# Optimization experiments

Hardware: AMD Instinct MI355X
Metric: run time of the kernel (lower is better)

## Reference

```python
import jax, jax.numpy as jnp
import numpy as np

N, E = 50000, 800000
IN_C, HID, OUT_C, HEADS = 256, 32, 16, 8
NEG_SLOPE = 0.2


def gat_conv(x, edge_index, W, att_src, att_dst, bias, heads, out_c, concat):
    """PyG-style GATConv (inference, dropout off, add_self_loops=True).

    x: [N, F_in], edge_index: [2, E] with row0=src(j), row1=dst(i).
    W: [F_in, heads*out_c], att_src/att_dst: [heads, out_c], bias: [heads*out_c] or [out_c].
    """
    n = x.shape[0]
    loops = jnp.arange(n, dtype=edge_index.dtype)
    src = jnp.concatenate([edge_index[0], loops])
    dst = jnp.concatenate([edge_index[1], loops])

    xl = (x @ W).reshape(n, heads, out_c)              # [N, H, C]
    a_src = jnp.einsum('nhc,hc->nh', xl, att_src)      # [N, H]
    a_dst = jnp.einsum('nhc,hc->nh', xl, att_dst)

    e = a_src[src] + a_dst[dst]                        # [E', H]
    e = jnp.where(e >= 0, e, NEG_SLOPE * e)            # leaky_relu
    e_max = jax.ops.segment_max(e, dst, num_segments=n)
    e_exp = jnp.exp(e - e_max[dst])
    denom = jax.ops.segment_sum(e_exp, dst, num_segments=n)
    alpha = e_exp / (denom[dst] + 1e-16)               # segment softmax over in-edges of dst

    msg = alpha[:, :, None] * xl[src]                  # [E', H, C]
    out = jax.ops.segment_sum(msg, dst, num_segments=n)  # [N, H, C]
    if concat:
        out = out.reshape(n, heads * out_c)
    else:
        out = out.mean(axis=1)
    return out + bias


def setup_inputs() -> dict:
    key = jax.random.key(0)
    ks = jax.random.split(key, 10)
    s_in = 1.0 / np.sqrt(IN_C)
    s_h = 1.0 / np.sqrt(HEADS * HID)
    x = jax.random.normal(ks[0], (N, IN_C), dtype=jnp.float32)
    edge_index = jax.random.randint(ks[1], (2, E), 0, N, dtype=jnp.int64)
    return {
        'x': x,
        'edge_index': edge_index,
        'W1': jax.random.normal(ks[2], (IN_C, HEADS * HID), dtype=jnp.float32) * s_in,
        'att_src1': jax.random.normal(ks[3], (HEADS, HID), dtype=jnp.float32) * s_h,
        'att_dst1': jax.random.normal(ks[4], (HEADS, HID), dtype=jnp.float32) * s_h,
        'b1': jnp.zeros((HEADS * HID,), dtype=jnp.float32),
        'W2': jax.random.normal(ks[5], (HEADS * HID, OUT_C), dtype=jnp.float32) * s_h,
        'att_src2': jax.random.normal(ks[6], (1, OUT_C), dtype=jnp.float32) * 0.1,
        'att_dst2': jax.random.normal(ks[7], (1, OUT_C), dtype=jnp.float32) * 0.1,
        'b2': jnp.zeros((OUT_C,), dtype=jnp.float32),
    }


def reference(x, edge_index, W1, att_src1, att_dst1, b1, W2, att_src2, att_dst2, b2):
    h = gat_conv(x, edge_index, W1, att_src1, att_dst1, b1, HEADS, HID, concat=True)
    h = jax.nn.relu(h)
    # F.dropout(training=False) is identity at inference
    out = gat_conv(h, edge_index, W2, att_src2, att_dst2, b2, 1, OUT_C, concat=False)
    return jax.nn.log_softmax(out, axis=1)
```

## Files before the change

### kernel.cpp

```cpp
#include <hip/hip_runtime.h>

#define IN_C 256
#define H1 8
#define C1 32
#define F1 256
#define OC 16
#define NEG 0.2f

typedef short short8 __attribute__((ext_vector_type(8)));
typedef unsigned short ushort8 __attribute__((ext_vector_type(8)));
typedef float floatx4 __attribute__((ext_vector_type(4)));

__device__ __forceinline__ unsigned short f2bf(float f) {
    unsigned u = __builtin_bit_cast(unsigned, f);
    u = (u + 0x7fffu + ((u >> 16) & 1u)) >> 16;
    return (unsigned short)u;
}
__device__ __forceinline__ float bf2f(unsigned short h) {
    unsigned u = ((unsigned)h) << 16;
    return __builtin_bit_cast(float, u);
}

__global__ __launch_bounds__(256) void k_fuse0(const int* __restrict__ ei,
                                               int* __restrict__ cnt,
                                               const float* __restrict__ W1,
                                               const float* __restrict__ W2,
                                               unsigned short* __restrict__ w1t,
                                               unsigned short* __restrict__ w2t, int E)
{
    int gid = blockIdx.x * 256 + threadIdx.x;
    if (gid < E) atomicAdd(&cnt[ei[E + gid]], 1);
    if (gid < 65536) {
        int n = gid >> 8, k = gid & 255;
        w1t[n * 256 + k] = f2bf(W1[k * 256 + n]);
    } else if (gid < 65536 + 4096) {
        int r = gid - 65536;
        int n = r >> 8, k = r & 255;
        w2t[n * 256 + k] = f2bf(W2[k * 16 + n]);
    }
}

__global__ __launch_bounds__(256) void k_gemm1(const float* __restrict__ A,
                                               const unsigned short* __restrict__ Bt,
                                               unsigned short* __restrict__ Cb, int M)
{
    __shared__ short As[128][40];
    __shared__ short Bs[128][40];
    const int tid  = threadIdx.x;
    const int lane = tid & 63;
    const int w    = tid >> 6;
    const int bm   = blockIdx.x * 128;
    const int bn   = blockIdx.y * 128;
    const int wm   = (w >> 1) * 64;
    const int wn   = (w & 1) * 64;
    const int srow = tid >> 1;
    const int soff = (tid & 1) * 16;
    floatx4 acc[4][4] = {};
    for (int k0 = 0; k0 < 256; k0 += 32) {
        __syncthreads();
        {
            int gr = bm + srow;
            float4 f0 = {0,0,0,0}, f1 = {0,0,0,0}, f2 = {0,0,0,0}, f3 = {0,0,0,0};
            if (gr < M) {
                const float4* p = (const float4*)(A + (size_t)gr * 256 + k0 + soff);
                f0 = p[0]; f1 = p[1]; f2 = p[2]; f3 = p[3];
            }
            ushort8 v0, v1;
            v0[0]=f2bf(f0.x); v0[1]=f2bf(f0.y); v0[2]=f2bf(f0.z); v0[3]=f2bf(f0.w);
            v0[4]=f2bf(f1.x); v0[5]=f2bf(f1.y); v0[6]=f2bf(f1.z); v0[7]=f2bf(f1.w);
            v1[0]=f2bf(f2.x); v1[1]=f2bf(f2.y); v1[2]=f2bf(f2.z); v1[3]=f2bf(f2.w);
            v1[4]=f2bf(f3.x); v1[5]=f2bf(f3.y); v1[6]=f2bf(f3.z); v1[7]=f2bf(f3.w);
            *(ushort8*)&As[srow][soff]     = v0;
            *(ushort8*)&As[srow][soff + 8] = v1;
        }
        {
            const ushort8* p = (const ushort8*)(Bt + (size_t)(bn + srow) * 256 + k0 + soff);
            *(ushort8*)&Bs[srow][soff]     = p[0];
            *(ushort8*)&Bs[srow][soff + 8] = p[1];
        }
        __syncthreads();
        short8 af[4], bf[4];
        const int q8 = (lane >> 4) * 8;
        const int l15 = lane & 15;
#pragma unroll
        for (int i = 0; i < 4; ++i) af[i] = *(const short8*)&As[wm + i * 16 + l15][q8];
#pragma unroll
        for (int j = 0; j < 4; ++j) bf[j] = *(const short8*)&Bs[wn + j * 16 + l15][q8];
#pragma unroll
        for (int i = 0; i < 4; ++i)
#pragma unroll
            for (int j = 0; j < 4; ++j)
                acc[i][j] = __builtin_amdgcn_mfma_f32_16x16x32_bf16(af[i], bf[j], acc[i][j], 0, 0, 0);
    }
    const int l15 = lane & 15;
    const int rq  = (lane >> 4) * 4;
#pragma unroll
    for (int i = 0; i < 4; ++i) {
#pragma unroll
        for (int reg = 0; reg < 4; ++reg) {
            int gr = bm + wm + i * 16 + rq + reg;
            if (gr < M) {
#pragma unroll
                for (int j = 0; j < 4; ++j)
                    Cb[(size_t)gr * 256 + bn + wn + j * 16 + l15] = f2bf(acc[i][j][reg]);
            }
        }
    }
}

__global__ __launch_bounds__(256) void k_att1(const unsigned short* __restrict__ xl,
                                              const float* __restrict__ att_s,
                                              const float* __restrict__ att_d,
                                              float* __restrict__ asrc,
                                              float* __restrict__ adst, int N)
{
    int idx = blockIdx.x * 256 + threadIdx.x;
    if (idx >= N * H1) return;
    int i = idx >> 3, h = idx & 7;
    const ushort4* xr = (const ushort4*)(xl + (size_t)i * F1 + h * C1);
    const float* s = att_s + h * C1;
    const float* d = att_d + h * C1;
    float s1 = 0.f, s2 = 0.f;
#pragma unroll
    for (int c4 = 0; c4 < 8; ++c4) {
        ushort4 v = xr[c4];
        float f0 = bf2f(v.x), f1 = bf2f(v.y), f2 = bf2f(v.z), f3 = bf2f(v.w);
        int c = c4 * 4;
        s1 += f0 * s[c] + f1 * s[c+1] + f2 * s[c+2] + f3 * s[c+3];
        s2 += f0 * d[c] + f1 * d[c+1] + f2 * d[c+2] + f3 * d[c+3];
    }
    asrc[idx] = s1; adst[idx] = s2;
}

__global__ __launch_bounds__(256) void k_scan_a(const int* __restrict__ cnt,
                                                int* __restrict__ rp,
                                                int* __restrict__ bsum, int N)
{
    __shared__ int ws4[4];
    int t = threadIdx.x, lane = t & 63, wid = t >> 6;
    int i = blockIdx.x * 256 + t;
    int v = (i < N) ? cnt[i] : 0;
    int incl = v;
#pragma unroll
    for (int off = 1; off < 64; off <<= 1) {
        int tv = __shfl_up(incl, off, 64);
        if (lane >= off) incl += tv;
    }
    if (lane == 63) ws4[wid] = incl;
    __syncthreads();
    int add = 0;
    for (int w = 0; w < wid; ++w) add += ws4[w];
    incl += add;
    if (i < N) rp[i + 1] = incl;
    if (t == 255) bsum[blockIdx.x] = incl;
}

__global__ __launch_bounds__(256) void k_scan_b(const int* __restrict__ bsum,
                                                int* __restrict__ boff, int NB)
{
    __shared__ int ws4[4];
    int t = threadIdx.x, lane = t & 63, wid = t >> 6;
    int i0 = t * 4;
    int v[4];
#pragma unroll
    for (int k = 0; k < 4; ++k) { int i = i0 + k; v[k] = (i < NB) ? bsum[i] : 0; }
    int s = v[0] + v[1] + v[2] + v[3];
    int incl = s;
#pragma unroll
    for (int off = 1; off < 64; off <<= 1) {
        int tv = __shfl_up(incl, off, 64);
        if (lane >= off) incl += tv;
    }
    if (lane == 63) ws4[wid] = incl;
    __syncthreads();
    int wpre = 0;
    for (int w = 0; w < wid; ++w) wpre += ws4[w];
    int run = wpre + incl - s;
#pragma unroll
    for (int k = 0; k < 4; ++k) {
        int i = i0 + k;
        if (i < NB) boff[i] = run;
        run += v[k];
    }
}

__global__ __launch_bounds__(256) void k_scan_c(int* __restrict__ rp,
                                                const int* __restrict__ boff,
                                                const int* __restrict__ cnt,
                                                int* __restrict__ cur, int N)
{
    int i = blockIdx.x * 256 + threadIdx.x;
    if (i < N) {
        int v = rp[i + 1] + boff[blockIdx.x];
        rp[i + 1] = v;
        cur[i] = v - cnt[i];
    }
    if (i == 0) rp[0] = 0;
}

__global__ __launch_bounds__(256) void k_scatter(const int* __restrict__ ei,
                                                 int* __restrict__ cur,
                                                 int* __restrict__ ssrc, int E)
{
    int e = blockIdx.x * 256 + threadIdx.x;
    if (e >= E) return;
    int s = ei[e];
    int d = ei[E + e];
    int pos = atomicAdd(&cur[d], 1);
    ssrc[pos] = s;
}

__global__ __launch_bounds__(256) void k_gather1(const int* __restrict__ rp,
                                                 const int* __restrict__ ssrc,
                                                 const unsigned short* __restrict__ xl,
                                                 const float* __restrict__ asrc,
                                                 const float* __restrict__ adst,
                                                 const float* __restrict__ bias,
                                                 unsigned short* __restrict__ hout, int N)
{
    int lane = threadIdx.x & 63;
    int node = blockIdx.x * 4 + (threadIdx.x >> 6);
    if (node >= N) return;
    int h  = lane >> 3;
    int cb = lane * 4;
    float ad = adst[(size_t)node * H1 + h];
    float e = asrc[(size_t)node * H1 + h] + ad;
    e = e >= 0.f ? e : NEG * e;
    float w = __expf(e);
    ushort4 xv = *(const ushort4*)(xl + (size_t)node * F1 + cb);
    float ax = w * bf2f(xv.x), ay = w * bf2f(xv.y), az = w * bf2f(xv.z), aw = w * bf2f(xv.w);
    float den = w;
    int jb = rp[node], je = rp[node + 1];
    int j = jb;
    for (; j + 4 <= je; j += 4) {
        int s0 = ssrc[j], s1 = ssrc[j+1], s2 = ssrc[j+2], s3 = ssrc[j+3];
        float e0 = asrc[(size_t)s0 * H1 + h] + ad;
        float e1 = asrc[(size_t)s1 * H1 + h] + ad;
        float e2 = asrc[(size_t)s2 * H1 + h] + ad;
        float e3 = asrc[(size_t)s3 * H1 + h] + ad;
        ushort4 r0 = *(const ushort4*)(xl + (size_t)s0 * F1 + cb);
        ushort4 r1 = *(const ushort4*)(xl + (size_t)s1 * F1 + cb);
        ushort4 r2 = *(const ushort4*)(xl + (size_t)s2 * F1 + cb);
        ushort4 r3 = *(const ushort4*)(xl + (size_t)s3 * F1 + cb);
        e0 = e0 >= 0.f ? e0 : NEG * e0;  float w0 = __expf(e0);
        e1 = e1 >= 0.f ? e1 : NEG * e1;  float w1 = __expf(e1);
        e2 = e2 >= 0.f ? e2 : NEG * e2;  float w2 = __expf(e2);
        e3 = e3 >= 0.f ? e3 : NEG * e3;  float w3 = __expf(e3);
        den += w0 + w1 + w2 + w3;
        ax += w0*bf2f(r0.x) + w1*bf2f(r1.x) + w2*bf2f(r2.x) + w3*bf2f(r3.x);
        ay += w0*bf2f(r0.y) + w1*bf2f(r1.y) + w2*bf2f(r2.y) + w3*bf2f(r3.y);
        az += w0*bf2f(r0.z) + w1*bf2f(r1.z) + w2*bf2f(r2.z) + w3*bf2f(r3.z);
        aw += w0*bf2f(r0.w) + w1*bf2f(r1.w) + w2*bf2f(r2.w) + w3*bf2f(r3.w);
    }
    for (; j < je; ++j) {
        int s = ssrc[j];
        float ev = asrc[(size_t)s * H1 + h] + ad;
        ev = ev >= 0.f ? ev : NEG * ev;
        float wv = __expf(ev);
        ushort4 sv = *(const ushort4*)(xl + (size_t)s * F1 + cb);
        ax += wv * bf2f(sv.x); ay += wv * bf2f(sv.y);
        az += wv * bf2f(sv.z); aw += wv * bf2f(sv.w);
        den += wv;
    }
    float inv = 1.f / (den + 1e-16f);
    float4 bv = *(const float4*)(bias + cb);
    ushort4 o;
    o.x = f2bf(fmaxf(ax * inv + bv.x, 0.f));
    o.y = f2bf(fmaxf(ay * inv + bv.y, 0.f));
    o.z = f2bf(fmaxf(az * inv + bv.z, 0.f));
    o.w = f2bf(fmaxf(aw * inv + bv.w, 0.f));
    *(ushort4*)(hout + (size_t)node * F1 + cb) = o;
}

__global__ __launch_bounds__(256) void k_gemm2(const unsigned short* __restrict__ Hm,
                                               const unsigned short* __restrict__ W2t,
                                               const float* __restrict__ as2,
                                               const float* __restrict__ ad2,
                                               unsigned short* __restrict__ xl2b,
                                               float* __restrict__ asrc,
                                               float* __restrict__ adst, int N)
{
    const int lane = threadIdx.x & 63;
    const int wid  = threadIdx.x >> 6;
    const int rowbase = blockIdx.x * 64 + wid * 16;
    const int col = lane & 15;
    const int q8  = (lane >> 4) * 8;
    const int m   = rowbase + col;
    const bool mv = m < N;
    const unsigned short* arow = Hm + (size_t)m * 256 + q8;
    const unsigned short* brow = W2t + (size_t)col * 256 + q8;
    floatx4 acc = {0.f, 0.f, 0.f, 0.f};
#pragma unroll
    for (int t = 0; t < 8; ++t) {
        short8 af = {0,0,0,0,0,0,0,0};
        if (mv) af = *(const short8*)(arow + t * 32);
        short8 bf = *(const short8*)(brow + t * 32);
        acc = __builtin_amdgcn_mfma_f32_16x16x32_bf16(af, bf, acc, 0, 0, 0);
    }
    float s_as = as2[col], s_ad = ad2[col];
    const int rq = (lane >> 4) * 4;
#pragma unroll
    for (int reg = 0; reg < 4; ++reg) {
        int row = rowbase + rq + reg;
        float v = acc[reg];
        float s1 = v * s_as, s2 = v * s_ad;
#pragma unroll
        for (int o = 1; o < 16; o <<= 1) { s1 += __shfl_xor(s1, o, 16); s2 += __shfl_xor(s2, o, 16); }
        if (row < N) {
            xl2b[(size_t)row * OC + col] = f2bf(v);
            if (col == 0) { asrc[row] = s1; adst[row] = s2; }
        }
    }
}

__global__ __launch_bounds__(256) void k_gather2(const int* __restrict__ rp,
                                                 const int* __restrict__ ssrc,
                                                 const unsigned short* __restrict__ xl2b,
                                                 const float* __restrict__ asrc,
                                                 const float* __restrict__ adst,
                                                 const float* __restrict__ bias,
                                                 float* __restrict__ out, int N)
{
    int sub  = threadIdx.x & 15;
    int node = blockIdx.x * 16 + (threadIdx.x >> 4);
    if (node >= N) return;
    float ad = adst[node];
    float e = asrc[node] + ad;
    e = e >= 0.f ? e : NEG * e;
    float w = __expf(e);
    float acc = w * bf2f(xl2b[(size_t)node * OC + sub]);
    float den = w;
    int jb = rp[node], je = rp[node + 1];
    int j = jb;
    for (; j + 4 <= je; j += 4) {
        int s0 = ssrc[j], s1i = ssrc[j+1], s2i = ssrc[j+2], s3i = ssrc[j+3];
        float e0 = asrc[s0] + ad, e1 = asrc[s1i] + ad, e2 = asrc[s2i] + ad, e3 = asrc[s3i] + ad;
        float v0 = bf2f(xl2b[(size_t)s0 * OC + sub]);
        float v1 = bf2f(xl2b[(size_t)s1i * OC + sub]);
        float v2 = bf2f(xl2b[(size_t)s2i * OC + sub]);
        float v3 = bf2f(xl2b[(size_t)s3i * OC + sub]);
        e0 = e0 >= 0.f ? e0 : NEG * e0;  float w0 = __expf(e0);
        e1 = e1 >= 0.f ? e1 : NEG * e1;  float w1 = __expf(e1);
        e2 = e2 >= 0.f ? e2 : NEG * e2;  float w2 = __expf(e2);
        e3 = e3 >= 0.f ? e3 : NEG * e3;  float w3 = __expf(e3);
        den += w0 + w1 + w2 + w3;
        acc += w0 * v0 + w1 * v1 + w2 * v2 + w3 * v3;
    }
    for (; j < je; ++j) {
        int s = ssrc[j];
        float ev = asrc[s] + ad;
        ev = ev >= 0.f ? ev : NEG * ev;
        float wv = __expf(ev);
        acc += wv * bf2f(xl2b[(size_t)s * OC + sub]);
        den += wv;
    }
    float v = acc / (den + 1e-16f) + bias[sub];
    float m = v;
#pragma unroll
    for (int o = 1; o < 16; o <<= 1) m = fmaxf(m, __shfl_xor(m, o, 16));
    float ex = __expf(v - m);
    float ss = ex;
#pragma unroll
    for (int o = 1; o < 16; o <<= 1) ss += __shfl_xor(ss, o, 16);
    out[(size_t)node * OC + sub] = v - m - logf(ss);
}

extern "C" void kernel_launch(void* const* d_in, const int* in_sizes, int n_in,
                              void* d_out, int out_size, void* d_ws, size_t ws_size,
                              hipStream_t stream)
{
    const float* x   = (const float*)d_in[0];
    const int*   ei  = (const int*)d_in[1];
    const float* W1  = (const float*)d_in[2];
    const float* as1 = (const float*)d_in[3];
    const float* ad1 = (const float*)d_in[4];
    const float* b1  = (const float*)d_in[5];
    const float* W2  = (const float*)d_in[6];
    const float* as2 = (const float*)d_in[7];
    const float* ad2 = (const float*)d_in[8];
    const float* b2  = (const float*)d_in[9];
    float* out = (float*)d_out;

    const int N = in_sizes[0] / IN_C;
    const int E = in_sizes[1] / 2;
    const int NB = (N + 255) / 256;

    char* base = (char*)d_ws;
    unsigned short* xl1b = (unsigned short*)base;
    unsigned short* hb   = xl1b + (size_t)N * F1;
    unsigned short* w1t  = hb + (size_t)N * F1;
    unsigned short* w2t  = w1t + 256 * 256;
    unsigned short* xl2b = w2t + 16 * 256;
    float* asrc1 = (float*)(xl2b + (size_t)N * OC);
    float* adst1 = asrc1 + (size_t)N * H1;
    float* asrc2 = adst1 + (size_t)N * H1;
    float* adst2 = asrc2 + N;
    int*   rp    = (int*)(adst2 + N);
    int*   cnt   = rp + (N + 1);
    int*   cur   = cnt + N;
    int*   bsum  = cur + N;
    int*   boff  = bsum + 1024;
    int*   ssrc  = boff + 1024;

    hipMemsetAsync(cnt, 0, (size_t)N * sizeof(int), stream);
    k_fuse0<<<(E + 255) / 256, 256, 0, stream>>>(ei, cnt, W1, W2, w1t, w2t, E);
    k_scan_a<<<NB, 256, 0, stream>>>(cnt, rp, bsum, N);
    k_scan_b<<<1, 256, 0, stream>>>(bsum, boff, NB);
    k_scan_c<<<NB, 256, 0, stream>>>(rp, boff, cnt, cur, N);
    k_scatter<<<(E + 255) / 256, 256, 0, stream>>>(ei, cur, ssrc, E);

    k_gemm1<<<dim3((N + 127) / 128, 2), 256, 0, stream>>>(x, w1t, xl1b, N);
    k_att1<<<(N * H1 + 255) / 256, 256, 0, stream>>>(xl1b, as1, ad1, asrc1, adst1, N);
    k_gather1<<<(N + 3) / 4, 256, 0, stream>>>(rp, ssrc, xl1b, asrc1, adst1, b1, hb, N);

    k_gemm2<<<(N + 63) / 64, 256, 0, stream>>>(hb, w2t, as2, ad2, xl2b, asrc2, adst2, N);
    k_gather2<<<(N + 15) / 16, 256, 0, stream>>>(rp, ssrc, xl2b, asrc2, adst2, b2, out, N);
}
```

Before: 333.5 us.

## Fuse attention-score dots into GEMM1 epilogue and split gather1 edges across half-waves

Drops the separate k_att1 kernel. The per-head source and destination attention dot products are now computed in the GEMM1 epilogue from fp32 accumulators, reduced with 16-lane xor shuffles, so the bf16 xl1 matrix is not re-read. Separately, gather1 now gives each half-wave alternate edges, with each lane loading 8 bf16 values (16 bytes) instead of 4, and combines the two halves with a cross-half shuffle at the end. This trades more epilogue shuffles and half-idle lanes on short neighbor lists for fewer kernel launches and wider, more parallel gather loads.

```diff
diff --git a/kernel.cpp b/kernel.cpp
--- a/kernel.cpp
+++ b/kernel.cpp
@@ -42,7 +42,11 @@
 
 __global__ __launch_bounds__(256) void k_gemm1(const float* __restrict__ A,
                                                const unsigned short* __restrict__ Bt,
-                                               unsigned short* __restrict__ Cb, int M)
+                                               const float* __restrict__ att_s,
+                                               const float* __restrict__ att_d,
+                                               unsigned short* __restrict__ Cb,
+                                               float* __restrict__ asrc,
+                                               float* __restrict__ adst, int M)
 {
     __shared__ short As[128][40];
     __shared__ short Bs[128][40];
@@ -81,11 +85,11 @@
         __syncthreads();
         short8 af[4], bf[4];
         const int q8 = (lane >> 4) * 8;
-        const int l15 = lane & 15;
-#pragma unroll
-        for (int i = 0; i < 4; ++i) af[i] = *(const short8*)&As[wm + i * 16 + l15][q8];
-#pragma unroll
-        for (int j = 0; j < 4; ++j) bf[j] = *(const short8*)&Bs[wn + j * 16 + l15][q8];
+        const int l15i = lane & 15;
+#pragma unroll
+        for (int i = 0; i < 4; ++i) af[i] = *(const short8*)&As[wm + i * 16 + l15i][q8];
+#pragma unroll
+        for (int j = 0; j < 4; ++j) bf[j] = *(const short8*)&Bs[wn + j * 16 + l15i][q8];
 #pragma unroll
         for (int i = 0; i < 4; ++i)
 #pragma unroll
@@ -94,42 +98,37 @@
     }
     const int l15 = lane & 15;
     const int rq  = (lane >> 4) * 4;
+    const int hA = (bn + wn) >> 5;
+    const int hB = hA + 1;
+    const float aS_A0 = att_s[hA * 32 + l15],      aS_A1 = att_s[hA * 32 + 16 + l15];
+    const float aS_B0 = att_s[hB * 32 + l15],      aS_B1 = att_s[hB * 32 + 16 + l15];
+    const float aD_A0 = att_d[hA * 32 + l15],      aD_A1 = att_d[hA * 32 + 16 + l15];
+    const float aD_B0 = att_d[hB * 32 + l15],      aD_B1 = att_d[hB * 32 + 16 + l15];
 #pragma unroll
     for (int i = 0; i < 4; ++i) {
 #pragma unroll
         for (int reg = 0; reg < 4; ++reg) {
             int gr = bm + wm + i * 16 + rq + reg;
+            float sA = acc[i][0][reg] * aS_A0 + acc[i][1][reg] * aS_A1;
+            float dA = acc[i][0][reg] * aD_A0 + acc[i][1][reg] * aD_A1;
+            float sB = acc[i][2][reg] * aS_B0 + acc[i][3][reg] * aS_B1;
+            float dB = acc[i][2][reg] * aD_B0 + acc[i][3][reg] * aD_B1;
+#pragma unroll
+            for (int o = 1; o < 16; o <<= 1) {
+                sA += __shfl_xor(sA, o, 16);  dA += __shfl_xor(dA, o, 16);
+                sB += __shfl_xor(sB, o, 16);  dB += __shfl_xor(dB, o, 16);
+            }
             if (gr < M) {
 #pragma unroll
                 for (int j = 0; j < 4; ++j)
                     Cb[(size_t)gr * 256 + bn + wn + j * 16 + l15] = f2bf(acc[i][j][reg]);
+                if (l15 == 0) {
+                    asrc[(size_t)gr * H1 + hA] = sA;  adst[(size_t)gr * H1 + hA] = dA;
+                    asrc[(size_t)gr * H1 + hB] = sB;  adst[(size_t)gr * H1 + hB] = dB;
+                }
             }
         }
     }
-}
-
-__global__ __launch_bounds__(256) void k_att1(const unsigned short* __restrict__ xl,
-                                              const float* __restrict__ att_s,
-                                              const float* __restrict__ att_d,
-                                              float* __restrict__ asrc,
-                                              float* __restrict__ adst, int N)
-{
-    int idx = blockIdx.x * 256 + threadIdx.x;
-    if (idx >= N * H1) return;
-    int i = idx >> 3, h = idx & 7;
-    const ushort4* xr = (const ushort4*)(xl + (size_t)i * F1 + h * C1);
-    const float* s = att_s + h * C1;
-    const float* d = att_d + h * C1;
-    float s1 = 0.f, s2 = 0.f;
-#pragma unroll
-    for (int c4 = 0; c4 < 8; ++c4) {
-        ushort4 v = xr[c4];
-        float f0 = bf2f(v.x), f1 = bf2f(v.y), f2 = bf2f(v.z), f3 = bf2f(v.w);
-        int c = c4 * 4;
-        s1 += f0 * s[c] + f1 * s[c+1] + f2 * s[c+2] + f3 * s[c+3];
-        s2 += f0 * d[c] + f1 * d[c+1] + f2 * d[c+2] + f3 * d[c+3];
-    }
-    asrc[idx] = s1; adst[idx] = s2;
 }
 
 __global__ __launch_bounds__(256) void k_scan_a(const int* __restrict__ cnt,
@@ -221,55 +220,77 @@
     int lane = threadIdx.x & 63;
     int node = blockIdx.x * 4 + (threadIdx.x >> 6);
     if (node >= N) return;
-    int h  = lane >> 3;
-    int cb = lane * 4;
+    int half = lane >> 5;
+    int l31  = lane & 31;
+    int c8   = l31 * 8;
+    int h    = l31 >> 2;
     float ad = adst[(size_t)node * H1 + h];
-    float e = asrc[(size_t)node * H1 + h] + ad;
-    e = e >= 0.f ? e : NEG * e;
-    float w = __expf(e);
-    ushort4 xv = *(const ushort4*)(xl + (size_t)node * F1 + cb);
-    float ax = w * bf2f(xv.x), ay = w * bf2f(xv.y), az = w * bf2f(xv.z), aw = w * bf2f(xv.w);
-    float den = w;
-    int jb = rp[node], je = rp[node + 1];
-    int j = jb;
-    for (; j + 4 <= je; j += 4) {
-        int s0 = ssrc[j], s1 = ssrc[j+1], s2 = ssrc[j+2], s3 = ssrc[j+3];
+
+    float4 a0 = {0,0,0,0}, a1 = {0,0,0,0};
+    float den = 0.f;
+
+    if (half == 0) {
+        float e = asrc[(size_t)node * H1 + h] + ad;
+        e = e >= 0.f ? e : NEG * e;
+        float w = __expf(e);
+        ushort8 r = *(const ushort8*)(xl + (size_t)node * F1 + c8);
+        a0.x += w*bf2f(r[0]); a0.y += w*bf2f(r[1]); a0.z += w*bf2f(r[2]); a0.w += w*bf2f(r[3]);
+        a1.x += w*bf2f(r[4]); a1.y += w*bf2f(r[5]); a1.z += w*bf2f(r[6]); a1.w += w*bf2f(r[7]);
+        den += w;
+    }
+
+    int jb = rp[node];
+    int Ecnt = rp[node + 1] - jb;
+    int k = half;
+    for (; k + 2 < Ecnt; k += 4) {
+        int s0 = ssrc[jb + k];
+        int s1 = ssrc[jb + k + 2];
         float e0 = asrc[(size_t)s0 * H1 + h] + ad;
         float e1 = asrc[(size_t)s1 * H1 + h] + ad;
-        float e2 = asrc[(size_t)s2 * H1 + h] + ad;
-        float e3 = asrc[(size_t)s3 * H1 + h] + ad;
-        ushort4 r0 = *(const ushort4*)(xl + (size_t)s0 * F1 + cb);
-        ushort4 r1 = *(const ushort4*)(xl + (size_t)s1 * F1 + cb);
-        ushort4 r2 = *(const ushort4*)(xl + (size_t)s2 * F1 + cb);
-        ushort4 r3 = *(const ushort4*)(xl + (size_t)s3 * F1 + cb);
+        ushort8 r0 = *(const ushort8*)(xl + (size_t)s0 * F1 + c8);
+        ushort8 r1 = *(const ushort8*)(xl + (size_t)s1 * F1 + c8);
         e0 = e0 >= 0.f ? e0 : NEG * e0;  float w0 = __expf(e0);
         e1 = e1 >= 0.f ? e1 : NEG * e1;  float w1 = __expf(e1);
-        e2 = e2 >= 0.f ? e2 : NEG * e2;  float w2 = __expf(e2);
-        e3 = e3 >= 0.f ? e3 : NEG * e3;  float w3 = __expf(e3);
-        den += w0 + w1 + w2 + w3;
-        ax += w0*bf2f(r0.x) + w1*bf2f(r1.x) + w2*bf2f(r2.x) + w3*bf2f(r3.x);
-        ay += w0*bf2f(r0.y) + w1*bf2f(r1.y) + w2*bf2f(r2.y) + w3*bf2f(r3.y);
-        az += w0*bf2f(r0.z) + w1*bf2f(r1.z) + w2*bf2f(r2.z) + w3*bf2f(r3.z);
-        aw += w0*bf2f(r0.w) + w1*bf2f(r1.w) + w2*bf2f(r2.w) + w3*bf2f(r3.w);
-    }
-    for (; j < je; ++j) {
-        int s = ssrc[j];
-        float ev = asrc[(size_t)s * H1 + h] + ad;
-        ev = ev >= 0.f ? ev : NEG * ev;
-        float wv = __expf(ev);
-        ushort4 sv = *(const ushort4*)(xl + (size_t)s * F1 + cb);
-        ax += wv * bf2f(sv.x); ay += wv * bf2f(sv.y);
-        az += wv * bf2f(sv.z); aw += wv * bf2f(sv.w);
-        den += wv;
-    }
-    float inv = 1.f / (den + 1e-16f);
-    float4 bv = *(const float4*)(bias + cb);
-    ushort4 o;
-    o.x = f2bf(fmaxf(ax * inv + bv.x, 0.f));
-    o.y = f2bf(fmaxf(ay * inv + bv.y, 0.f));
-    o.z = f2bf(fmaxf(az * inv + bv.z, 0.f));
-    o.w = f2bf(fmaxf(aw * inv + bv.w, 0.f));
-    *(ushort4*)(hout + (size_t)node * F1 + cb) = o;
+        den += w0 + w1;
+        a0.x += w0*bf2f(r0[0]) + w1*bf2f(r1[0]);
+        a0.y += w0*bf2f(r0[1]) + w1*bf2f(r1[1]);
+        a0.z += w0*bf2f(r0[2]) + w1*bf2f(r1[2]);
+        a0.w += w0*bf2f(r0[3]) + w1*bf2f(r1[3]);
+        a1.x += w0*bf2f(r0[4]) + w1*bf2f(r1[4]);
+        a1.y += w0*bf2f(r0[5]) + w1*bf2f(r1[5]);
+        a1.z += w0*bf2f(r0[6]) + w1*bf2f(r1[6]);
+        a1.w += w0*bf2f(r0[7]) + w1*bf2f(r1[7]);
+    }
+    if (k < Ecnt) {
+        int s = ssrc[jb + k];
+        float e = asrc[(size_t)s * H1 + h] + ad;
+        e = e >= 0.f ? e : NEG * e;
+        float w = __expf(e);
+        ushort8 r = *(const ushort8*)(xl + (size_t)s * F1 + c8);
+        den += w;
+        a0.x += w*bf2f(r[0]); a0.y += w*bf2f(r[1]); a0.z += w*bf2f(r[2]); a0.w += w*bf2f(r[3]);
+        a1.x += w*bf2f(r[4]); a1.y += w*bf2f(r[5]); a1.z += w*bf2f(r[6]); a1.w += w*bf2f(r[7]);
+    }
+    a0.x += __shfl_xor(a0.x, 32);  a0.y += __shfl_xor(a0.y, 32);
+    a0.z += __shfl_xor(a0.z, 32);  a0.w += __shfl_xor(a0.w, 32);
+    a1.x += __shfl_xor(a1.x, 32);  a1.y += __shfl_xor(a1.y, 32);
+    a1.z += __shfl_xor(a1.z, 32);  a1.w += __shfl_xor(a1.w, 32);
+    den  += __shfl_xor(den, 32);
+    if (half == 0) {
+        float inv = 1.f / (den + 1e-16f);
+        const float4* bv = (const float4*)(bias + c8);
+        float4 b0 = bv[0], b1 = bv[1];
+        ushort8 o;
+        o[0] = f2bf(fmaxf(a0.x * inv + b0.x, 0.f));
+        o[1] = f2bf(fmaxf(a0.y * inv + b0.y, 0.f));
+        o[2] = f2bf(fmaxf(a0.z * inv + b0.z, 0.f));
+        o[3] = f2bf(fmaxf(a0.w * inv + b0.w, 0.f));
+        o[4] = f2bf(fmaxf(a1.x * inv + b1.x, 0.f));
+        o[5] = f2bf(fmaxf(a1.y * inv + b1.y, 0.f));
+        o[6] = f2bf(fmaxf(a1.z * inv + b1.z, 0.f));
+        o[7] = f2bf(fmaxf(a1.w * inv + b1.w, 0.f));
+        *(ushort8*)(hout + (size_t)node * F1 + c8) = o;
+    }
 }
 
 __global__ __launch_bounds__(256) void k_gemm2(const unsigned short* __restrict__ Hm,
@@ -409,8 +430,7 @@
     k_scan_c<<<NB, 256, 0, stream>>>(rp, boff, cnt, cur, N);
     k_scatter<<<(E + 255) / 256, 256, 0, stream>>>(ei, cur, ssrc, E);
 
-    k_gemm1<<<dim3((N + 127) / 128, 2), 256, 0, stream>>>(x, w1t, xl1b, N);
-    k_att1<<<(N * H1 + 255) / 256, 256, 0, stream>>>(xl1b, as1, ad1, asrc1, adst1, N);
+    k_gemm1<<<dim3((N + 127) / 128, 2), 256, 0, stream>>>(x, w1t, as1, ad1, xl1b, asrc1, adst1, N);
     k_gather1<<<(N + 3) / 4, 256, 0, stream>>>(rp, ssrc, xl1b, asrc1, adst1, b1, hb, N);
 
     k_gemm2<<<(N + 63) / 64, 256, 0, stream>>>(hb, w2t, as2, ad2, xl2b, asrc2, adst2, N);
```

Measured after the change: 322.4 us. 1.03x faster.

## Fuse attention logits into GEMM1 and store layer-1 features as FP8

Applied to the files above, without the earlier changes.

GEMM1 now covers all 256 output columns per block, with B read straight from global memory instead of staged in LDS. It computes the per-head source and destination attention dot products in its epilogue through 16-lane shuffle reductions, which removes the separate k_att1 kernel and its extra pass over xl. The xl features are stored as FP8 instead of bf16, halving the bytes gathered per edge in gather1. The trade-offs are lower precision in the aggregated features (attention logits stay fp32), a larger accumulator footprint per wave, and unstaged global B loads.

```diff
diff --git a/kernel.cpp b/kernel.cpp
--- a/kernel.cpp
+++ b/kernel.cpp
@@ -19,6 +19,14 @@
 __device__ __forceinline__ float bf2f(unsigned short h) {
     unsigned u = ((unsigned)h) << 16;
     return __builtin_bit_cast(float, u);
+}
+__device__ __forceinline__ unsigned char f2fp8(float f) {
+    int p = __builtin_amdgcn_cvt_pk_fp8_f32(f, f, 0, false);
+    return (unsigned char)(p & 0xff);
+}
+template <int SEL>
+__device__ __forceinline__ float fp82f(unsigned int dw) {
+    return __builtin_amdgcn_cvt_f32_fp8(dw, SEL);
 }
 
 __global__ __launch_bounds__(256) void k_fuse0(const int* __restrict__ ei,
@@ -40,22 +48,104 @@
     }
 }
 
+__global__ __launch_bounds__(256) void k_scan_a(const int* __restrict__ cnt,
+                                                int* __restrict__ rp,
+                                                int* __restrict__ bsum, int N)
+{
+    __shared__ int ws4[4];
+    int t = threadIdx.x, lane = t & 63, wid = t >> 6;
+    int i = blockIdx.x * 256 + t;
+    int v = (i < N) ? cnt[i] : 0;
+    int incl = v;
+#pragma unroll
+    for (int off = 1; off < 64; off <<= 1) {
+        int tv = __shfl_up(incl, off, 64);
+        if (lane >= off) incl += tv;
+    }
+    if (lane == 63) ws4[wid] = incl;
+    __syncthreads();
+    int add = 0;
+    for (int w = 0; w < wid; ++w) add += ws4[w];
+    incl += add;
+    if (i < N) rp[i + 1] = incl;
+    if (t == 255) bsum[blockIdx.x] = incl;
+}
+
+__global__ __launch_bounds__(256) void k_scan_b(const int* __restrict__ bsum,
+                                                int* __restrict__ boff, int NB)
+{
+    __shared__ int ws4[4];
+    int t = threadIdx.x, lane = t & 63, wid = t >> 6;
+    int i0 = t * 4;
+    int v[4];
+#pragma unroll
+    for (int k = 0; k < 4; ++k) { int i = i0 + k; v[k] = (i < NB) ? bsum[i] : 0; }
+    int s = v[0] + v[1] + v[2] + v[3];
+    int incl = s;
+#pragma unroll
+    for (int off = 1; off < 64; off <<= 1) {
+        int tv = __shfl_up(incl, off, 64);
+        if (lane >= off) incl += tv;
+    }
+    if (lane == 63) ws4[wid] = incl;
+    __syncthreads();
+    int wpre = 0;
+    for (int w = 0; w < wid; ++w) wpre += ws4[w];
+    int run = wpre + incl - s;
+#pragma unroll
+    for (int k = 0; k < 4; ++k) {
+        int i = i0 + k;
+        if (i < NB) boff[i] = run;
+        run += v[k];
+    }
+}
+
+__global__ __launch_bounds__(256) void k_scan_c(int* __restrict__ rp,
+                                                const int* __restrict__ boff,
+                                                const int* __restrict__ cnt,
+                                                int* __restrict__ cur, int N)
+{
+    int i = blockIdx.x * 256 + threadIdx.x;
+    if (i < N) {
+        int v = rp[i + 1] + boff[blockIdx.x];
+        rp[i + 1] = v;
+        cur[i] = v - cnt[i];
+    }
+    if (i == 0) rp[0] = 0;
+}
+
+__global__ __launch_bounds__(256) void k_scatter(const int* __restrict__ ei,
+                                                 int* __restrict__ cur,
+                                                 int* __restrict__ ssrc, int E)
+{
+    int e = blockIdx.x * 256 + threadIdx.x;
+    if (e >= E) return;
+    int s = ei[e];
+    int d = ei[E + e];
+    int pos = atomicAdd(&cur[d], 1);
+    ssrc[pos] = s;
+}
+
 __global__ __launch_bounds__(256) void k_gemm1(const float* __restrict__ A,
                                                const unsigned short* __restrict__ Bt,
-                                               unsigned short* __restrict__ Cb, int M)
+                                               const float* __restrict__ att_s,
+                                               const float* __restrict__ att_d,
+                                               unsigned char* __restrict__ C8,
+                                               float* __restrict__ asrc,
+                                               float* __restrict__ adst, int M)
 {
     __shared__ short As[128][40];
-    __shared__ short Bs[128][40];
     const int tid  = threadIdx.x;
     const int lane = tid & 63;
     const int w    = tid >> 6;
     const int bm   = blockIdx.x * 128;
-    const int bn   = blockIdx.y * 128;
     const int wm   = (w >> 1) * 64;
-    const int wn   = (w & 1) * 64;
+    const int wn   = (w & 1) * 128;
     const int srow = tid >> 1;
     const int soff = (tid & 1) * 16;
-    floatx4 acc[4][4] = {};
+    const int q8   = (lane >> 4) * 8;
+    const int l15  = lane & 15;
+    floatx4 acc[4][8] = {};
     for (int k0 = 0; k0 < 256; k0 += 32) {
         __syncthreads();
         {
@@ -73,27 +163,27 @@
             *(ushort8*)&As[srow][soff]     = v0;
             *(ushort8*)&As[srow][soff + 8] = v1;
         }
-        {
-            const ushort8* p = (const ushort8*)(Bt + (size_t)(bn + srow) * 256 + k0 + soff);
-            *(ushort8*)&Bs[srow][soff]     = p[0];
-            *(ushort8*)&Bs[srow][soff + 8] = p[1];
+        __syncthreads();
+        short8 af[4];
+#pragma unroll
+        for (int i = 0; i < 4; ++i) af[i] = *(const short8*)&As[wm + i * 16 + l15][q8];
+#pragma unroll
+        for (int j = 0; j < 8; ++j) {
+            short8 bf = *(const short8*)(Bt + (size_t)(wn + j * 16 + l15) * 256 + k0 + q8);
+#pragma unroll
+            for (int i = 0; i < 4; ++i)
+                acc[i][j] = __builtin_amdgcn_mfma_f32_16x16x32_bf16(af[i], bf, acc[i][j], 0, 0, 0);
         }
-        __syncthreads();
-        short8 af[4], bf[4];
-        const int q8 = (lane >> 4) * 8;
-        const int l15 = lane & 15;
-#pragma unroll
-        for (int i = 0; i < 4; ++i) af[i] = *(const short8*)&As[wm + i * 16 + l15][q8];
-#pragma unroll
-        for (int j = 0; j < 4; ++j) bf[j] = *(const short8*)&Bs[wn + j * 16 + l15][q8];
-#pragma unroll
-        for (int i = 0; i < 4; ++i)
-#pragma unroll
-            for (int j = 0; j < 4; ++j)
-                acc[i][j] = __builtin_amdgcn_mfma_f32_16x16x32_bf16(af[i], bf[j], acc[i][j], 0, 0, 0);
-    }
-    const int l15 = lane & 15;
+    }
     const int rq  = (lane >> 4) * 4;
+    const int hb0 = wn >> 5;
+    float aS0[4], aS1[4], aD0[4], aD1[4];
+#pragma unroll
+    for (int hl = 0; hl < 4; ++hl) {
+        int hh = hb0 + hl;
+        aS0[hl] = att_s[hh * 32 + l15];  aS1[hl] = att_s[hh * 32 + 16 + l15];
+        aD0[hl] = att_d[hh * 32 + l15];  aD1[hl] = att_d[hh * 32 + 16 + l15];
+    }
 #pragma unroll
     for (int i = 0; i < 4; ++i) {
 #pragma unroll
@@ -101,118 +191,30 @@
             int gr = bm + wm + i * 16 + rq + reg;
             if (gr < M) {
 #pragma unroll
-                for (int j = 0; j < 4; ++j)
-                    Cb[(size_t)gr * 256 + bn + wn + j * 16 + l15] = f2bf(acc[i][j][reg]);
+                for (int j = 0; j < 8; ++j)
+                    C8[(size_t)gr * 256 + wn + j * 16 + l15] = f2fp8(acc[i][j][reg]);
+            }
+#pragma unroll
+            for (int hl = 0; hl < 4; ++hl) {
+                float s = acc[i][2*hl][reg] * aS0[hl] + acc[i][2*hl+1][reg] * aS1[hl];
+                float d = acc[i][2*hl][reg] * aD0[hl] + acc[i][2*hl+1][reg] * aD1[hl];
+#pragma unroll
+                for (int o = 1; o < 16; o <<= 1) {
+                    s += __shfl_xor(s, o, 16);
+                    d += __shfl_xor(d, o, 16);
+                }
+                if (gr < M && l15 == 0) {
+                    asrc[(size_t)gr * H1 + hb0 + hl] = s;
+                    adst[(size_t)gr * H1 + hb0 + hl] = d;
+                }
             }
         }
     }
 }
 
-__global__ __launch_bounds__(256) void k_att1(const unsigned short* __restrict__ xl,
-                                              const float* __restrict__ att_s,
-                                              const float* __restrict__ att_d,
-                                              float* __restrict__ asrc,
-                                              float* __restrict__ adst, int N)
-{
-    int idx = blockIdx.x * 256 + threadIdx.x;
-    if (idx >= N * H1) return;
-    int i = idx >> 3, h = idx & 7;
-    const ushort4* xr = (const ushort4*)(xl + (size_t)i * F1 + h * C1);
-    const float* s = att_s + h * C1;
-    const float* d = att_d + h * C1;
-    float s1 = 0.f, s2 = 0.f;
-#pragma unroll
-    for (int c4 = 0; c4 < 8; ++c4) {
-        ushort4 v = xr[c4];
-        float f0 = bf2f(v.x), f1 = bf2f(v.y), f2 = bf2f(v.z), f3 = bf2f(v.w);
-        int c = c4 * 4;
-        s1 += f0 * s[c] + f1 * s[c+1] + f2 * s[c+2] + f3 * s[c+3];
-        s2 += f0 * d[c] + f1 * d[c+1] + f2 * d[c+2] + f3 * d[c+3];
-    }
-    asrc[idx] = s1; adst[idx] = s2;
-}
-
-__global__ __launch_bounds__(256) void k_scan_a(const int* __restrict__ cnt,
-                                                int* __restrict__ rp,
-                                                int* __restrict__ bsum, int N)
-{
-    __shared__ int ws4[4];
-    int t = threadIdx.x, lane = t & 63, wid = t >> 6;
-    int i = blockIdx.x * 256 + t;
-    int v = (i < N) ? cnt[i] : 0;
-    int incl = v;
-#pragma unroll
-    for (int off = 1; off < 64; off <<= 1) {
-        int tv = __shfl_up(incl, off, 64);
-        if (lane >= off) incl += tv;
-    }
-    if (lane == 63) ws4[wid] = incl;
-    __syncthreads();
-    int add = 0;
-    for (int w = 0; w < wid; ++w) add += ws4[w];
-    incl += add;
-    if (i < N) rp[i + 1] = incl;
-    if (t == 255) bsum[blockIdx.x] = incl;
-}
-
-__global__ __launch_bounds__(256) void k_scan_b(const int* __restrict__ bsum,
-                                                int* __restrict__ boff, int NB)
-{
-    __shared__ int ws4[4];
-    int t = threadIdx.x, lane = t & 63, wid = t >> 6;
-    int i0 = t * 4;
-    int v[4];
-#pragma unroll
-    for (int k = 0; k < 4; ++k) { int i = i0 + k; v[k] = (i < NB) ? bsum[i] : 0; }
-    int s = v[0] + v[1] + v[2] + v[3];
-    int incl = s;
-#pragma unroll
-    for (int off = 1; off < 64; off <<= 1) {
-        int tv = __shfl_up(incl, off, 64);
-        if (lane >= off) incl += tv;
-    }
-    if (lane == 63) ws4[wid] = incl;
-    __syncthreads();
-    int wpre = 0;
-    for (int w = 0; w < wid; ++w) wpre += ws4[w];
-    int run = wpre + incl - s;
-#pragma unroll
-    for (int k = 0; k < 4; ++k) {
-        int i = i0 + k;
-        if (i < NB) boff[i] = run;
-        run += v[k];
-    }
-}
-
-__global__ __launch_bounds__(256) void k_scan_c(int* __restrict__ rp,
-                                                const int* __restrict__ boff,
-                                                const int* __restrict__ cnt,
-                                                int* __restrict__ cur, int N)
-{
-    int i = blockIdx.x * 256 + threadIdx.x;
-    if (i < N) {
-        int v = rp[i + 1] + boff[blockIdx.x];
-        rp[i + 1] = v;
-        cur[i] = v - cnt[i];
-    }
-    if (i == 0) rp[0] = 0;
-}
-
-__global__ __launch_bounds__(256) void k_scatter(const int* __restrict__ ei,
-                                                 int* __restrict__ cur,
-                                                 int* __restrict__ ssrc, int E)
-{
-    int e = blockIdx.x * 256 + threadIdx.x;
-    if (e >= E) return;
-    int s = ei[e];
-    int d = ei[E + e];
-    int pos = atomicAdd(&cur[d], 1);
-    ssrc[pos] = s;
-}
-
 __global__ __launch_bounds__(256) void k_gather1(const int* __restrict__ rp,
                                                  const int* __restrict__ ssrc,
-                                                 const unsigned short* __restrict__ xl,
+                                                 const unsigned char* __restrict__ xl8,
                                                  const float* __restrict__ asrc,
                                                  const float* __restrict__ adst,
                                                  const float* __restrict__ bias,
@@ -227,8 +229,9 @@
     float e = asrc[(size_t)node * H1 + h] + ad;
     e = e >= 0.f ? e : NEG * e;
     float w = __expf(e);
-    ushort4 xv = *(const ushort4*)(xl + (size_t)node * F1 + cb);
-    float ax = w * bf2f(xv.x), ay = w * bf2f(xv.y), az = w * bf2f(xv.z), aw = w * bf2f(xv.w);
+    unsigned int xv = *(const unsigned int*)(xl8 + (size_t)node * F1 + cb);
+    float ax = w * fp82f<0>(xv), ay = w * fp82f<1>(xv);
+    float az = w * fp82f<2>(xv), aw = w * fp82f<3>(xv);
     float den = w;
     int jb = rp[node], je = rp[node + 1];
     int j = jb;
@@ -238,28 +241,28 @@
         float e1 = asrc[(size_t)s1 * H1 + h] + ad;
         float e2 = asrc[(size_t)s2 * H1 + h] + ad;
         float e3 = asrc[(size_t)s3 * H1 + h] + ad;
-        ushort4 r0 = *(const ushort4*)(xl + (size_t)s0 * F1 + cb);
-        ushort4 r1 = *(const ushort4*)(xl + (size_t)s1 * F1 + cb);
-        ushort4 r2 = *(const ushort4*)(xl + (size_t)s2 * F1 + cb);
-        ushort4 r3 = *(const ushort4*)(xl + (size_t)s3 * F1 + cb);
+        unsigned int r0 = *(const unsigned int*)(xl8 + (size_t)s0 * F1 + cb);
+        unsigned int r1 = *(const unsigned int*)(xl8 + (size_t)s1 * F1 + cb);
+        unsigned int r2 = *(const unsigned int*)(xl8 + (size_t)s2 * F1 + cb);
+        unsigned int r3 = *(const unsigned int*)(xl8 + (size_t)s3 * F1 + cb);
         e0 = e0 >= 0.f ? e0 : NEG * e0;  float w0 = __expf(e0);
         e1 = e1 >= 0.f ? e1 : NEG * e1;  float w1 = __expf(e1);
         e2 = e2 >= 0.f ? e2 : NEG * e2;  float w2 = __expf(e2);
         e3 = e3 >= 0.f ? e3 : NEG * e3;  float w3 = __expf(e3);
         den += w0 + w1 + w2 + w3;
-        ax += w0*bf2f(r0.x) + w1*bf2f(r1.x) + w2*bf2f(r2.x) + w3*bf2f(r3.x);
-        ay += w0*bf2f(r0.y) + w1*bf2f(r1.y) + w2*bf2f(r2.y) + w3*bf2f(r3.y);
-        az += w0*bf2f(r0.z) + w1*bf2f(r1.z) + w2*bf2f(r2.z) + w3*bf2f(r3.z);
-        aw += w0*bf2f(r0.w) + w1*bf2f(r1.w) + w2*bf2f(r2.w) + w3*bf2f(r3.w);
+        ax += w0*fp82f<0>(r0) + w1*fp82f<0>(r1) + w2*fp82f<0>(r2) + w3*fp82f<0>(r3);
+        ay += w0*fp82f<1>(r0) + w1*fp82f<1>(r1) + w2*fp82f<1>(r2) + w3*fp82f<1>(r3);
+        az += w0*fp82f<2>(r0) + w1*fp82f<2>(r1) + w2*fp82f<2>(r2) + w3*fp82f<2>(r3);
+        aw += w0*fp82f<3>(r0) + w1*fp82f<3>(r1) + w2*fp82f<3>(r2) + w3*fp82f<3>(r3);
     }
     for (; j < je; ++j) {
         int s = ssrc[j];
         float ev = asrc[(size_t)s * H1 + h] + ad;
         ev = ev >= 0.f ? ev : NEG * ev;
         float wv = __expf(ev);
-        ushort4 sv = *(const ushort4*)(xl + (size_t)s * F1 + cb);
-        ax += wv * bf2f(sv.x); ay += wv * bf2f(sv.y);
-        az += wv * bf2f(sv.z); aw += wv * bf2f(sv.w);
+        unsigned int r = *(const unsigned int*)(xl8 + (size_t)s * F1 + cb);
+        ax += wv * fp82f<0>(r); ay += wv * fp82f<1>(r);
+        az += wv * fp82f<2>(r); aw += wv * fp82f<3>(r);
         den += wv;
     }
     float inv = 1.f / (den + 1e-16f);
@@ -386,8 +389,8 @@
     const int NB = (N + 255) / 256;
 
     char* base = (char*)d_ws;
-    unsigned short* xl1b = (unsigned short*)base;
-    unsigned short* hb   = xl1b + (size_t)N * F1;
+    unsigned char*  xl8  = (unsigned char*)base;
+    unsigned short* hb   = (unsigned short*)(xl8 + (size_t)N * F1);
     unsigned short* w1t  = hb + (size_t)N * F1;
     unsigned short* w2t  = w1t + 256 * 256;
     unsigned short* xl2b = w2t + 16 * 256;
@@ -402,16 +405,15 @@
     int*   boff  = bsum + 1024;
     int*   ssrc  = boff + 1024;
 
-    hipMemsetAsync(cnt, 0, (size_t)N * sizeof(int), stream);
+    (void)hipMemsetAsync(cnt, 0, (size_t)N * sizeof(int), stream);
     k_fuse0<<<(E + 255) / 256, 256, 0, stream>>>(ei, cnt, W1, W2, w1t, w2t, E);
     k_scan_a<<<NB, 256, 0, stream>>>(cnt, rp, bsum, N);
     k_scan_b<<<1, 256, 0, stream>>>(bsum, boff, NB);
     k_scan_c<<<NB, 256, 0, stream>>>(rp, boff, cnt, cur, N);
     k_scatter<<<(E + 255) / 256, 256, 0, stream>>>(ei, cur, ssrc, E);
 
-    k_gemm1<<<dim3((N + 127) / 128, 2), 256, 0, stream>>>(x, w1t, xl1b, N);
-    k_att1<<<(N * H1 + 255) / 256, 256, 0, stream>>>(xl1b, as1, ad1, asrc1, adst1, N);
-    k_gather1<<<(N + 3) / 4, 256, 0, stream>>>(rp, ssrc, xl1b, asrc1, adst1, b1, hb, N);
+    k_gemm1<<<(N + 127) / 128, 256, 0, stream>>>(x, w1t, as1, ad1, xl8, asrc1, adst1, N);
+    k_gather1<<<(N + 3) / 4, 256, 0, stream>>>(rp, ssrc, xl8, asrc1, adst1, b1, hb, N);
 
     k_gemm2<<<(N + 63) / 64, 256, 0, stream>>>(hb, w2t, as2, ad2, xl2b, asrc2, adst2, N);
     k_gather2<<<(N + 15) / 16, 256, 0, stream>>>(rp, ssrc, xl2b, asrc2, adst2, b2, out, N);
```

New measurement: 327.4 us. No clear change (-1.9%).
